# Performance work log

Hardware: AMD Instinct MI355X
Metric: run time of the kernel (lower is better)

## Reference

```python
import jax, jax.numpy as jnp
import numpy as np

H = 1024   # hdim
D = 200    # linear_first bottleneck (fixed in source)
K = 8      # len(token_ids)
B = 8
L = 4096


def setup_inputs() -> dict:
    key = jax.random.key(0)
    ks = jax.random.split(key, 7)
    hidd_states = jax.random.normal(ks[0], (B, L, H), dtype=jnp.float32)
    prompt_types = jax.random.randint(ks[1], (B,), 0, 3, dtype=jnp.int32)
    ner_labels = jax.random.randint(ks[2], (B, L), 0, K, dtype=jnp.int32)
    # learned params (PyTorch Linear default-ish init scale)
    W1 = jax.random.normal(ks[3], (H, D), dtype=jnp.float32) / np.sqrt(H)
    b1 = jnp.zeros((D,), dtype=jnp.float32)
    W2 = jax.random.normal(ks[4], (D, K), dtype=jnp.float32) / np.sqrt(D)
    b2 = jnp.zeros((K,), dtype=jnp.float32)
    return {"hidd_states": hidd_states, "W1": W1, "b1": b1, "W2": W2,
            "b2": b2, "prompt_types": prompt_types, "ner_labels": ner_labels}


def _det_output(hidd, W1, b1, W2, b2, prompt_types):
    # hidd: [B, L, H]
    # attn = linear_second(tanh(linear_first(h)))  -> [B, L, K]
    attn = jnp.tanh(jnp.einsum('blh,hd->bld', hidd, W1) + b1)
    attn = jnp.einsum('bld,dk->blk', attn, W2) + b2
    # bmm(attn[:, :, None], h[:, None, :]).mean(dim=2) == attn * mean_h(h)
    m = jnp.mean(hidd, axis=-1)            # [B, L]
    s = attn * m[..., None]                # [B, L, K]
    Lf = s.shape[1]
    # prefix: running mean over t <= j
    pre = jnp.cumsum(s, axis=1) / jnp.arange(1, Lf + 1, dtype=s.dtype)[:, None]
    # postfix: running mean over t >= j (reverse cumsum)
    rev = jnp.flip(jnp.cumsum(jnp.flip(s, axis=1), axis=1), axis=1)
    post = rev / (Lf - jnp.arange(Lf, dtype=s.dtype))[:, None]
    # other: per-token, no mean over dim 0
    pt = prompt_types[:, None, None]
    det = jnp.where(pt == 0, pre, jnp.where(pt == 1, post, s))  # [B, L, K]
    return det


def reference(hidd_states, W1, b1, W2, b2, prompt_types, ner_labels):
    det = _det_output(hidd_states, W1, b1, W2, b2, prompt_types)
    ner_preds = jax.nn.softmax(det, axis=-1)                     # [B, L, K]
    # CrossEntropyLoss applied (as in the repo) to the softmax probs:
    logp = jax.nn.log_softmax(ner_preds, axis=-1)                # [B, L, K]
    picked = jnp.take_along_axis(logp, ner_labels[..., None].astype(jnp.int32), axis=-1)[..., 0]
    losses = -jnp.mean(picked, axis=1)                           # [B]
    return losses
```

## Files before the change

kernel.cpp:

```cpp
#include <hip/hip_runtime.h>
#include <hip/hip_bf16.h>
#include <math.h>

#define H   1024
#define Dd  200
#define Kc  8
#define Bb  8
#define Ll  4096
#define Mm  (Bb*Ll)

typedef __attribute__((ext_vector_type(8))) short short8;
typedef __attribute__((ext_vector_type(4))) float f32x4;

#define OFF_W1T  0
#define OFF_S    425984
#define OFF_SEG  (OFF_S + Mm*Kc*4)
#define OFF_PART (OFF_SEG + Bb*16*Kc*4)
#define WS_NEEDED (OFF_PART + 128*4)

#define GLOAD16(g, l) __builtin_amdgcn_global_load_lds( \
    (const __attribute__((address_space(1))) void*)(g),  \
    (__attribute__((address_space(3))) void*)(l), 16, 0, 0)

__device__ __forceinline__ unsigned short f2bf(float x){
  unsigned u = __float_as_uint(x);
  unsigned r = (u + 0x7FFFu + ((u >> 16) & 1u)) >> 16;
  return (unsigned short)r;
}

__global__ __launch_bounds__(256) void prep_w1t(const float* __restrict__ W1,
                                                unsigned short* __restrict__ W1T){
  int idx = blockIdx.x * 256 + threadIdx.x;
  int d = idx >> 10;
  int h = idx & 1023;
  float v = (d < Dd) ? W1[h * Dd + d] : 0.f;
  W1T[idx] = f2bf(v);
}

__global__ __launch_bounds__(512) __attribute__((amdgpu_waves_per_eu(4)))
void gemm_fused(const float* __restrict__ hidd,
                const unsigned short* __restrict__ W1T,
                const float* __restrict__ b1,
                const float* __restrict__ W2,
                const float* __restrict__ b2,
                float* __restrict__ sOut){
  __shared__ char lB[2 * 32768];
  __shared__ float epart[8][4][4][8];
  __shared__ float lrow[64];

  const int tid  = threadIdx.x;
  const int lane = tid & 63;
  const int wid  = tid >> 6;
  const int lc   = lane & 15;
  const int lg   = lane >> 4;
  const int wr   = wid >> 1;
  const int wc   = wid & 1;
  const int t0   = wc * 7;
  const int ntw  = 7 - wc;
  const long rowBase = (long)blockIdx.x * 64;

  const float* ap = hidd + (size_t)(rowBase + wr * 16 + lc) * H + lg * 8;

  const int swz = (((lane & 7) ^ (lane >> 3)) & 7) * 16;
  const char* bsrcj[4];
  #pragma unroll
  for (int j = 0; j < 4; ++j){
    int colj = wid * 32 + j * 8 + (lane >> 3);
    colj = (colj < 207) ? colj : 207;
    bsrcj[j] = (const char*)W1T + (size_t)colj * 2048 + swz;
  }

  float4 pf[4];
  #pragma unroll
  for (int x = 0; x < 4; ++x)
    pf[x] = *(const float4*)(ap + (x >> 1) * 32 + (x & 1) * 4);
  #pragma unroll
  for (int j = 0; j < 4; ++j)
    GLOAD16(bsrcj[j], &lB[wid * 4096 + j * 1024]);

  f32x4 acc[7];
  #pragma unroll
  for (int t = 0; t < 7; ++t) acc[t] = (f32x4){0.f, 0.f, 0.f, 0.f};
  float ms = 0.f;

  #pragma unroll 2
  for (int kt = 0; kt < 16; ++kt){
    const int cur = kt & 1, nxt = cur ^ 1;

    asm volatile("s_waitcnt vmcnt(4)" ::: "memory");
    const float4 a0 = pf[0], a1 = pf[1], a2 = pf[2], a3 = pf[3];
    ms += a0.x + a0.y + a0.z + a0.w + a1.x + a1.y + a1.z + a1.w
        + a2.x + a2.y + a2.z + a2.w + a3.x + a3.y + a3.z + a3.w;
    union Uc { short8 s8; __hip_bfloat162 h2[4]; };
    Uc u0, u1;
    u0.h2[0] = __float22bfloat162_rn(make_float2(a0.x, a0.y));
    u0.h2[1] = __float22bfloat162_rn(make_float2(a0.z, a0.w));
    u0.h2[2] = __float22bfloat162_rn(make_float2(a1.x, a1.y));
    u0.h2[3] = __float22bfloat162_rn(make_float2(a1.z, a1.w));
    u1.h2[0] = __float22bfloat162_rn(make_float2(a2.x, a2.y));
    u1.h2[1] = __float22bfloat162_rn(make_float2(a2.z, a2.w));
    u1.h2[2] = __float22bfloat162_rn(make_float2(a3.x, a3.y));
    u1.h2[3] = __float22bfloat162_rn(make_float2(a3.z, a3.w));

    if (kt < 15){
      #pragma unroll
      for (int x = 0; x < 4; ++x)
        pf[x] = *(const float4*)(ap + (kt + 1) * 64 + (x >> 1) * 32 + (x & 1) * 4);
      #pragma unroll
      for (int j = 0; j < 4; ++j)
        GLOAD16(bsrcj[j] + (kt + 1) * 128, &lB[nxt * 32768 + wid * 4096 + j * 1024]);
      asm volatile("s_waitcnt vmcnt(8)" ::: "memory");
    } else {
      asm volatile("s_waitcnt vmcnt(0)" ::: "memory");
    }
    __builtin_amdgcn_s_barrier();
    __builtin_amdgcn_sched_barrier(0);

    const char* bb = &lB[cur * 32768];
    #pragma unroll
    for (int tt = 0; tt < 7; ++tt){
      if (tt < ntw){
        const int col = (t0 + tt) * 16 + lc;
        const int cs  = (col & 7) * 16;
        const short8 bf0 = *(const short8*)(bb + col * 128 + (( 0 + lg * 16) ^ cs));
        const short8 bf1 = *(const short8*)(bb + col * 128 + ((64 + lg * 16) ^ cs));
        acc[tt] = __builtin_amdgcn_mfma_f32_16x16x32_bf16(u0.s8, bf0, acc[tt], 0, 0, 0);
        acc[tt] = __builtin_amdgcn_mfma_f32_16x16x32_bf16(u1.s8, bf1, acc[tt], 0, 0, 0);
      }
    }
    if (kt < 15){
      __builtin_amdgcn_sched_barrier(0);
      __builtin_amdgcn_s_barrier();
      __builtin_amdgcn_sched_barrier(0);
    }
  }

  ms += __shfl_xor(ms, 16);
  ms += __shfl_xor(ms, 32);
  if (wc == 0 && lane < 16) lrow[wr * 16 + lane] = ms * (1.0f / 1024.0f);

  float part[4][Kc];
  #pragma unroll
  for (int r = 0; r < 4; ++r)
    #pragma unroll
    for (int k = 0; k < Kc; ++k) part[r][k] = 0.f;

  #pragma unroll
  for (int tt = 0; tt < 7; ++tt){
    if (tt < ntw){
      const int col = (t0 + tt) * 16 + lc;
      float b1v = 0.f;
      float w2v[Kc];
      if (col < Dd){
        b1v = b1[col];
        const float4 wa = *(const float4*)(W2 + col * Kc);
        const float4 wb = *(const float4*)(W2 + col * Kc + 4);
        w2v[0] = wa.x; w2v[1] = wa.y; w2v[2] = wa.z; w2v[3] = wa.w;
        w2v[4] = wb.x; w2v[5] = wb.y; w2v[6] = wb.z; w2v[7] = wb.w;
      } else {
        #pragma unroll
        for (int k = 0; k < Kc; ++k) w2v[k] = 0.f;
      }
      #pragma unroll
      for (int r = 0; r < 4; ++r){
        const float a = tanhf(acc[tt][r] + b1v);
        #pragma unroll
        for (int k = 0; k < Kc; ++k) part[r][k] = fmaf(a, w2v[k], part[r][k]);
      }
    }
  }
  #pragma unroll
  for (int m = 1; m < 16; m <<= 1){
    #pragma unroll
    for (int r = 0; r < 4; ++r)
      #pragma unroll
      for (int k = 0; k < Kc; ++k)
        part[r][k] += __shfl_xor(part[r][k], m);
  }
  if ((lane & 15) == 0){
    #pragma unroll
    for (int r = 0; r < 4; ++r)
      #pragma unroll
      for (int k = 0; k < Kc; ++k)
        epart[wid][lg][r][k] = part[r][k];
  }
  __syncthreads();

  {
    const int row2 = tid >> 3, k = tid & 7;
    const int wr2 = row2 >> 4, lg2 = (row2 >> 2) & 3, r2 = row2 & 3;
    const float v = epart[wr2 * 2][lg2][r2][k] + epart[wr2 * 2 + 1][lg2][r2][k];
    sOut[(size_t)(rowBase + row2) * Kc + k] = (v + b2[k]) * lrow[row2];
  }
}

__global__ __launch_bounds__(256) void seg_sum(const float* __restrict__ s,
                                               float* __restrict__ segs){
  int b   = blockIdx.x >> 4;
  int seg = blockIdx.x & 15;
  int tid = threadIdx.x, lane = tid & 63, wid = tid >> 6;
  int l = seg * 256 + tid;
  const float4* sp = (const float4*)(s + ((long)(b * Ll + l)) * Kc);
  float4 v0 = sp[0], v1 = sp[1];
  float v[8] = {v0.x, v0.y, v0.z, v0.w, v1.x, v1.y, v1.z, v1.w};
  #pragma unroll
  for (int k = 0; k < 8; ++k){
    float x = v[k];
    x += __shfl_xor(x, 1);  x += __shfl_xor(x, 2);  x += __shfl_xor(x, 4);
    x += __shfl_xor(x, 8);  x += __shfl_xor(x, 16); x += __shfl_xor(x, 32);
    v[k] = x;
  }
  __shared__ float part[4][8];
  if (lane == 0){
    #pragma unroll
    for (int k = 0; k < 8; ++k) part[wid][k] = v[k];
  }
  __syncthreads();
  if (tid < 8){
    float t = part[0][tid] + part[1][tid] + part[2][tid] + part[3][tid];
    segs[(b * 16 + seg) * 8 + tid] = t;
  }
}

__global__ __launch_bounds__(256) void scan_loss(const float* __restrict__ s,
                                                 const float* __restrict__ segs,
                                                 const int* __restrict__ ptypes,
                                                 const int* __restrict__ labels,
                                                 float* __restrict__ partial){
  int b   = blockIdx.x >> 4;
  int seg = blockIdx.x & 15;
  int tid = threadIdx.x, lane = tid & 63, wid = tid >> 6;
  int l = seg * 256 + tid;

  float carry[8], T[8];
  #pragma unroll
  for (int k = 0; k < 8; ++k){ carry[k] = 0.f; T[k] = 0.f; }
  for (int ss = 0; ss < 16; ++ss){
    #pragma unroll
    for (int k = 0; k < 8; ++k){
      float x = segs[(b * 16 + ss) * 8 + k];
      T[k] += x;
      if (ss < seg) carry[k] += x;
    }
  }

  const float4* sp = (const float4*)(s + ((long)(b * Ll + l)) * Kc);
  float4 v0 = sp[0], v1 = sp[1];
  float sv[8] = {v0.x, v0.y, v0.z, v0.w, v1.x, v1.y, v1.z, v1.w};
  float P[8];
  #pragma unroll
  for (int k = 0; k < 8; ++k) P[k] = sv[k];

  #pragma unroll
  for (int st = 1; st < 64; st <<= 1){
    #pragma unroll
    for (int k = 0; k < 8; ++k){
      float u = __shfl_up(P[k], st);
      if (lane >= st) P[k] += u;
    }
  }
  __shared__ float wsum[4][8];
  if (lane == 63){
    #pragma unroll
    for (int k = 0; k < 8; ++k) wsum[wid][k] = P[k];
  }
  __syncthreads();
  for (int w = 0; w < wid; ++w){
    #pragma unroll
    for (int k = 0; k < 8; ++k) P[k] += wsum[w][k];
  }
  #pragma unroll
  for (int k = 0; k < 8; ++k) P[k] += carry[k];

  int pt = ptypes[b];
  float det[8];
  if (pt == 0){
    float inv = 1.0f / (float)(l + 1);
    #pragma unroll
    for (int k = 0; k < 8; ++k) det[k] = P[k] * inv;
  } else if (pt == 1){
    float inv = 1.0f / (float)(Ll - l);
    #pragma unroll
    for (int k = 0; k < 8; ++k) det[k] = (T[k] - P[k] + sv[k]) * inv;
  } else {
    #pragma unroll
    for (int k = 0; k < 8; ++k) det[k] = sv[k];
  }

  float mx = det[0];
  #pragma unroll
  for (int k = 1; k < 8; ++k) mx = fmaxf(mx, det[k]);
  float e[8], Z = 0.f;
  #pragma unroll
  for (int k = 0; k < 8; ++k){ e[k] = expf(det[k] - mx); Z += e[k]; }
  float invZ = 1.0f / Z;
  float p[8];
  #pragma unroll
  for (int k = 0; k < 8; ++k) p[k] = e[k] * invZ;
  float mx2 = p[0];
  #pragma unroll
  for (int k = 1; k < 8; ++k) mx2 = fmaxf(mx2, p[k]);
  float Z2 = 0.f;
  #pragma unroll
  for (int k = 0; k < 8; ++k) Z2 += expf(p[k] - mx2);
  float lse = logf(Z2) + mx2;

  int lab = labels[b * Ll + l];
  float picked = 0.f;
  #pragma unroll
  for (int k = 0; k < 8; ++k) picked = (lab == k) ? (p[k] - lse) : picked;

  float a = picked;
  a += __shfl_xor(a, 1);  a += __shfl_xor(a, 2);  a += __shfl_xor(a, 4);
  a += __shfl_xor(a, 8);  a += __shfl_xor(a, 16); a += __shfl_xor(a, 32);
  __shared__ float red[4];
  if (lane == 0) red[wid] = a;
  __syncthreads();
  if (tid == 0){
    partial[blockIdx.x] = red[0] + red[1] + red[2] + red[3];
  }
}

__global__ __launch_bounds__(128) void final_loss(const float* __restrict__ partial,
                                                  float* __restrict__ out){
  int tid = threadIdx.x;
  float v = partial[tid];
  v += __shfl_xor(v, 1); v += __shfl_xor(v, 2);
  v += __shfl_xor(v, 4); v += __shfl_xor(v, 8);
  if ((tid & 15) == 0) out[tid >> 4] = -v * (1.0f / (float)Ll);
}

extern "C" void kernel_launch(void* const* d_in, const int* in_sizes, int n_in,
                              void* d_out, int out_size, void* d_ws, size_t ws_size,
                              hipStream_t stream){
  const float* hidd  = (const float*)d_in[0];
  const float* W1    = (const float*)d_in[1];
  const float* b1    = (const float*)d_in[2];
  const float* W2    = (const float*)d_in[3];
  const float* b2    = (const float*)d_in[4];
  const int* ptypes  = (const int*)d_in[5];
  const int* labels  = (const int*)d_in[6];
  float* out = (float*)d_out;
  char* ws = (char*)d_ws;
  if (ws_size < (size_t)WS_NEEDED) return;

  unsigned short* W1T = (unsigned short*)(ws + OFF_W1T);
  float* s       = (float*)(ws + OFF_S);
  float* segs    = (float*)(ws + OFF_SEG);
  float* partial = (float*)(ws + OFF_PART);

  prep_w1t<<<(208 * H) / 256, 256, 0, stream>>>(W1, W1T);
  gemm_fused<<<Mm / 64, 512, 0, stream>>>(hidd, W1T, b1, W2, b2, s);
  seg_sum<<<Bb * 16, 256, 0, stream>>>(s, segs);
  scan_loss<<<Bb * 16, 256, 0, stream>>>(s, segs, ptypes, labels, partial);
  final_loss<<<1, 128, 0, stream>>>(partial, out);
}
```

Measured before the change: 237.4 us.

## Stage A tile through LDS so each hidden-state element is loaded once per block

Previously each of the two column-half waves loaded and converted the same A rows (fp32 hidden states) from global memory, so the A tile was read twice per block. Now each thread loads one 8-float chunk, converts it to bf16, and writes it into a swizzled LDS tile, which the MFMA waves then read back as fragments. Row-mean accumulation moves to a per-thread partial reduced over 8 lanes, and the B fragment offsets are precomputed. The cost is an extra LDS write, an lgkmcnt wait and a barrier dependency on A every k-step, and a single-buffered A tile.

```diff
diff --git a/kernel.cpp b/kernel.cpp
--- a/kernel.cpp
+++ b/kernel.cpp
@@ -27,6 +27,8 @@
   unsigned r = (u + 0x7FFFu + ((u >> 16) & 1u)) >> 16;
   return (unsigned short)r;
 }
+
+union Uc { short8 s8; __hip_bfloat162 h2[4]; };
 
 __global__ __launch_bounds__(256) void prep_w1t(const float* __restrict__ W1,
                                                 unsigned short* __restrict__ W1T){
@@ -44,9 +46,11 @@
                 const float* __restrict__ W2,
                 const float* __restrict__ b2,
                 float* __restrict__ sOut){
+  __shared__ char lA[64 * 128];
   __shared__ char lB[2 * 32768];
   __shared__ float epart[8][4][4][8];
   __shared__ float lrow[64];
+  char* lAc = lA;
 
   const int tid  = threadIdx.x;
   const int lane = tid & 63;
@@ -59,7 +63,9 @@
   const int ntw  = 7 - wc;
   const long rowBase = (long)blockIdx.x * 64;
 
-  const float* ap = hidd + (size_t)(rowBase + wr * 16 + lc) * H + lg * 8;
+  const int arow = tid >> 3, ak8 = tid & 7;
+  const float* ag = hidd + (size_t)(rowBase + arow) * H + ak8 * 8;
+  const int awb = ((arow * 128 + ak8 * 16) ^ ((arow & 7) << 4));
 
   const int swz = (((lane & 7) ^ (lane >> 3)) & 7) * 16;
   const char* bsrcj[4];
@@ -70,10 +76,22 @@
     bsrcj[j] = (const char*)W1T + (size_t)colj * 2048 + swz;
   }
 
-  float4 pf[4];
-  #pragma unroll
-  for (int x = 0; x < 4; ++x)
-    pf[x] = *(const float4*)(ap + (x >> 1) * 32 + (x & 1) * 4);
+  const int acs   = (lc & 7) << 4;
+  const int aoff0 = (wr * 16 + lc) * 128 + ((lg * 16) ^ acs);
+  const int aoff1 = (wr * 16 + lc) * 128 + (((64 + lg * 16)) ^ acs);
+
+  int boff0[7], boff1[7];
+  #pragma unroll
+  for (int tt = 0; tt < 7; ++tt){
+    const int col = (t0 + tt) * 16 + lc;
+    const int cs  = (col & 7) * 16;
+    boff0[tt] = col * 128 + ((lg * 16) ^ cs);
+    boff1[tt] = col * 128 + ((64 + lg * 16) ^ cs);
+  }
+
+  float4 pf[2][2];
+  pf[0][0] = *(const float4*)(ag);
+  pf[0][1] = *(const float4*)(ag + 4);
   #pragma unroll
   for (int j = 0; j < 4; ++j)
     GLOAD16(bsrcj[j], &lB[wid * 4096 + j * 1024]);
@@ -83,61 +101,61 @@
   for (int t = 0; t < 7; ++t) acc[t] = (f32x4){0.f, 0.f, 0.f, 0.f};
   float ms = 0.f;
 
-  #pragma unroll 2
-  for (int kt = 0; kt < 16; ++kt){
-    const int cur = kt & 1, nxt = cur ^ 1;
-
-    asm volatile("s_waitcnt vmcnt(4)" ::: "memory");
-    const float4 a0 = pf[0], a1 = pf[1], a2 = pf[2], a3 = pf[3];
-    ms += a0.x + a0.y + a0.z + a0.w + a1.x + a1.y + a1.z + a1.w
-        + a2.x + a2.y + a2.z + a2.w + a3.x + a3.y + a3.z + a3.w;
-    union Uc { short8 s8; __hip_bfloat162 h2[4]; };
-    Uc u0, u1;
-    u0.h2[0] = __float22bfloat162_rn(make_float2(a0.x, a0.y));
-    u0.h2[1] = __float22bfloat162_rn(make_float2(a0.z, a0.w));
-    u0.h2[2] = __float22bfloat162_rn(make_float2(a1.x, a1.y));
-    u0.h2[3] = __float22bfloat162_rn(make_float2(a1.z, a1.w));
-    u1.h2[0] = __float22bfloat162_rn(make_float2(a2.x, a2.y));
-    u1.h2[1] = __float22bfloat162_rn(make_float2(a2.z, a2.w));
-    u1.h2[2] = __float22bfloat162_rn(make_float2(a3.x, a3.y));
-    u1.h2[3] = __float22bfloat162_rn(make_float2(a3.z, a3.w));
-
-    if (kt < 15){
-      #pragma unroll
-      for (int x = 0; x < 4; ++x)
-        pf[x] = *(const float4*)(ap + (kt + 1) * 64 + (x >> 1) * 32 + (x & 1) * 4);
-      #pragma unroll
-      for (int j = 0; j < 4; ++j)
-        GLOAD16(bsrcj[j] + (kt + 1) * 128, &lB[nxt * 32768 + wid * 4096 + j * 1024]);
-      asm volatile("s_waitcnt vmcnt(8)" ::: "memory");
-    } else {
-      asm volatile("s_waitcnt vmcnt(0)" ::: "memory");
-    }
-    __builtin_amdgcn_s_barrier();
-    __builtin_amdgcn_sched_barrier(0);
-
-    const char* bb = &lB[cur * 32768];
-    #pragma unroll
-    for (int tt = 0; tt < 7; ++tt){
-      if (tt < ntw){
-        const int col = (t0 + tt) * 16 + lc;
-        const int cs  = (col & 7) * 16;
-        const short8 bf0 = *(const short8*)(bb + col * 128 + (( 0 + lg * 16) ^ cs));
-        const short8 bf1 = *(const short8*)(bb + col * 128 + ((64 + lg * 16) ^ cs));
-        acc[tt] = __builtin_amdgcn_mfma_f32_16x16x32_bf16(u0.s8, bf0, acc[tt], 0, 0, 0);
-        acc[tt] = __builtin_amdgcn_mfma_f32_16x16x32_bf16(u1.s8, bf1, acc[tt], 0, 0, 0);
-      }
-    }
-    if (kt < 15){
-      __builtin_amdgcn_sched_barrier(0);
-      __builtin_amdgcn_s_barrier();
-      __builtin_amdgcn_sched_barrier(0);
-    }
-  }
-
-  ms += __shfl_xor(ms, 16);
-  ms += __shfl_xor(ms, 32);
-  if (wc == 0 && lane < 16) lrow[wr * 16 + lane] = ms * (1.0f / 1024.0f);
+#define GEMM_STEP(KT, CUR, NXT) do {                                           \
+    if ((KT) < 15){                                                            \
+      pf[NXT][0] = *(const float4*)(ag + ((KT) + 1) * 64);                     \
+      pf[NXT][1] = *(const float4*)(ag + ((KT) + 1) * 64 + 4);                 \
+      GLOAD16(bsrcj[0] + ((KT)+1)*128, &lB[(NXT)*32768 + wid*4096 + 0*1024]);  \
+      GLOAD16(bsrcj[1] + ((KT)+1)*128, &lB[(NXT)*32768 + wid*4096 + 1*1024]);  \
+      GLOAD16(bsrcj[2] + ((KT)+1)*128, &lB[(NXT)*32768 + wid*4096 + 2*1024]);  \
+      GLOAD16(bsrcj[3] + ((KT)+1)*128, &lB[(NXT)*32768 + wid*4096 + 3*1024]);  \
+      asm volatile("s_waitcnt vmcnt(6)" ::: "memory");                         \
+    } else {                                                                   \
+      asm volatile("s_waitcnt vmcnt(0)" ::: "memory");                         \
+    }                                                                          \
+    {                                                                          \
+      const float4 a0 = pf[CUR][0], a1 = pf[CUR][1];                           \
+      ms += a0.x + a0.y + a0.z + a0.w + a1.x + a1.y + a1.z + a1.w;             \
+      Uc u;                                                                    \
+      u.h2[0] = __float22bfloat162_rn(make_float2(a0.x, a0.y));                \
+      u.h2[1] = __float22bfloat162_rn(make_float2(a0.z, a0.w));                \
+      u.h2[2] = __float22bfloat162_rn(make_float2(a1.x, a1.y));                \
+      u.h2[3] = __float22bfloat162_rn(make_float2(a1.z, a1.w));                \
+      *(short8*)(lAc + awb) = u.s8;                                            \
+    }                                                                          \
+    asm volatile("s_waitcnt lgkmcnt(0)" ::: "memory");                         \
+    __builtin_amdgcn_s_barrier();                                              \
+    __builtin_amdgcn_sched_barrier(0);                                         \
+    {                                                                          \
+      const short8 af0 = *(const short8*)(lAc + aoff0);                        \
+      const short8 af1 = *(const short8*)(lAc + aoff1);                        \
+      const char* bb = &lB[(CUR) * 32768];                                     \
+      _Pragma("unroll")                                                        \
+      for (int tt = 0; tt < 7; ++tt){                                          \
+        if (tt < ntw){                                                         \
+          const short8 bf0 = *(const short8*)(bb + boff0[tt]);                 \
+          const short8 bf1 = *(const short8*)(bb + boff1[tt]);                 \
+          acc[tt] = __builtin_amdgcn_mfma_f32_16x16x32_bf16(af0, bf0, acc[tt], 0, 0, 0); \
+          acc[tt] = __builtin_amdgcn_mfma_f32_16x16x32_bf16(af1, bf1, acc[tt], 0, 0, 0); \
+        }                                                                      \
+      }                                                                        \
+    }                                                                          \
+    if ((KT) < 15){                                                            \
+      __builtin_amdgcn_sched_barrier(0);                                       \
+      __builtin_amdgcn_s_barrier();                                            \
+      __builtin_amdgcn_sched_barrier(0);                                       \
+    }                                                                          \
+  } while (0)
+
+  for (int m = 0; m < 8; ++m){
+    const int kt0 = m * 2;
+    GEMM_STEP(kt0, 0, 1);
+    GEMM_STEP(kt0 + 1, 1, 0);
+  }
+#undef GEMM_STEP
+
+  ms += __shfl_xor(ms, 1); ms += __shfl_xor(ms, 2); ms += __shfl_xor(ms, 4);
+  if ((tid & 7) == 0) lrow[tid >> 3] = ms * (1.0f / 1024.0f);
 
   float part[4][Kc];
   #pragma unroll
```

Result: faster. 229.9 us (-3.2%).
